# Optimization experiments

Measured on AMD Instinct MI355X. Metric: run time of the kernel, lower is better.

## Reference

```python
import jax, jax.numpy as jnp
import numpy as np

B, T, DIM, HEADS, DH = 4, 2048, 1024, 16, 64  # dh = dim // heads


def setup_inputs() -> dict:
    key = jax.random.key(0)
    k1, k2, k3 = jax.random.split(key, 3)
    x = jax.random.normal(k1, (B, T, DIM), dtype=jnp.float32)
    # nn.Linear weights, stored as [in, out] for x @ W convention
    W_qkv = jax.random.normal(k2, (DIM, 3 * HEADS * DH), dtype=jnp.float32) * (DIM ** -0.5)
    W_o = jax.random.normal(k3, (HEADS * DH, DIM), dtype=jnp.float32) * ((HEADS * DH) ** -0.5)
    return {"x": x, "W_qkv": W_qkv, "W_o": W_o}


def reference(x, W_qkv, W_o):
    b, t, _ = x.shape
    qkv = x @ W_qkv  # [b, t, 3*h*dh]
    # einops 'b t (d k h) -> k b h t d' with k=3, h=HEADS: fused axis splits as (dh, 3, h)
    qkv = qkv.reshape(b, t, DH, 3, HEADS)
    qkv = jnp.transpose(qkv, (3, 0, 4, 1, 2))  # [3, b, h, t, dh]
    q, k, v = qkv[0], qkv[1], qkv[2]
    scale = DH ** -0.5
    scores = jnp.einsum('bhid,bhjd->bhij', q, k) * scale  # [b, h, t, t]
    attn = jax.nn.softmax(scores, axis=-1)
    out = jnp.einsum('bhij,bhjd->bhid', attn, v)  # [b, h, t, dh]
    out = jnp.transpose(out, (0, 2, 1, 3)).reshape(b, t, HEADS * DH)  # 'b h t d -> b t (h d)'
    return out @ W_o
```

## Files before the change

### kernel.cpp

```cpp
#include <hip/hip_runtime.h>

typedef __bf16 bf16;
typedef __bf16 bf16x2 __attribute__((ext_vector_type(2)));
typedef __bf16 bf16x4 __attribute__((ext_vector_type(4)));
typedef __bf16 bf16x8 __attribute__((ext_vector_type(8)));
typedef float  f32x4  __attribute__((ext_vector_type(4)));
typedef unsigned int u32;
typedef unsigned int u32x2 __attribute__((ext_vector_type(2)));
typedef unsigned int u32x4 __attribute__((ext_vector_type(4)));

#define LOG2E 1.44269504088896340736f
#define EXP_SC (0.125f * LOG2E)

#if __has_builtin(__builtin_amdgcn_exp2f)
#define EXP2F(x) __builtin_amdgcn_exp2f(x)
#else
#define EXP2F(x) __builtin_exp2f(x)
#endif

__device__ __forceinline__ u32 pk_bf16(float lo, float hi) {
  u32 a = __float_as_uint(lo) + 0x8000u;
  u32 b = __float_as_uint(hi) + 0x8000u;
  return __builtin_amdgcn_perm(b, a, 0x07060302);
}
#if __has_builtin(__builtin_amdgcn_cvt_pk_bf16_f32)
__device__ __forceinline__ u32 cvtpk(float lo, float hi) {
  bf16x2 t = __builtin_amdgcn_cvt_pk_bf16_f32(lo, hi);
  return __builtin_bit_cast(u32, t);
}
#else
__device__ __forceinline__ u32 cvtpk(float lo, float hi) { return pk_bf16(lo, hi); }
#endif
__device__ __forceinline__ unsigned short bf16r(float x) {
  return (unsigned short)((__float_as_uint(x) + 0x8000u) >> 16);
}

__device__ __forceinline__ void async_ld16(void* lds, const void* g) {
  __builtin_amdgcn_global_load_lds(
      (const __attribute__((address_space(1))) void*)(g),
      (__attribute__((address_space(3))) void*)(lds),
      16, 0, 0);
}

__global__ void prep_all(const float* __restrict__ x,    bf16* __restrict__ xb,
                         const float* __restrict__ Wqkv, bf16* __restrict__ wqkvT,
                         const float* __restrict__ Wo,   bf16* __restrict__ woT) {
  __shared__ float s[12288];
  const int bid = blockIdx.x;
  const int tid = threadIdx.x;
  if (bid < 8192) {
    int i = bid * 256 + tid;
    float4 v = ((const float4*)x)[i];
    u32x2 o = { pk_bf16(v.x, v.y), pk_bf16(v.z, v.w) };
    *(u32x2*)(xb + (size_t)i * 4) = o;
  } else if (bid < 8448) {
    const int k0 = (bid - 8192) * 4;
    for (int i = tid; i < 3072; i += 256) {
      int r = i / 768, c = (i - r * 768) * 4;
      *(float4*)(s + r * 3072 + c) = *(const float4*)(Wqkv + (size_t)(k0 + r) * 3072 + c);
    }
    __syncthreads();
    for (int n = tid; n < 3072; n += 256) {
      int d = n & 63, h = (n >> 6) & 15, wch = n >> 10;
      int on = d * 48 + wch * 16 + h;
      u32x2 v = { pk_bf16(s[0 * 3072 + on], s[1 * 3072 + on]),
                  pk_bf16(s[2 * 3072 + on], s[3 * 3072 + on]) };
      *(u32x2*)(wqkvT + (size_t)n * 1024 + k0) = v;
    }
  } else {
    const int k0 = (bid - 8448) * 8;
    for (int i = tid; i < 2048; i += 256) {
      int r = i >> 8, c = (i & 255) * 4;
      *(float4*)(s + r * 1024 + c) = *(const float4*)(Wo + (size_t)(k0 + r) * 1024 + c);
    }
    __syncthreads();
    for (int n = tid; n < 1024; n += 256) {
      u32x4 v = { pk_bf16(s[0 * 1024 + n], s[1 * 1024 + n]),
                  pk_bf16(s[2 * 1024 + n], s[3 * 1024 + n]),
                  pk_bf16(s[4 * 1024 + n], s[5 * 1024 + n]),
                  pk_bf16(s[6 * 1024 + n], s[7 * 1024 + n]) };
      *(u32x4*)(woT + (size_t)n * 1024 + k0) = v;
    }
  }
}

template <int MODE>
__launch_bounds__(256, 2)
__global__ void gemm_bt(const bf16* __restrict__ A, const bf16* __restrict__ BT,
                        float* __restrict__ C, int N,
                        bf16* __restrict__ Qb, bf16* __restrict__ Kb, bf16* __restrict__ Vb) {
  constexpr int K = 1024;
  __shared__ bf16 sA[128 * 64];
  __shared__ bf16 sB[128 * 64];
  const int m0 = blockIdx.x * 128;
  const int n0 = blockIdx.y * 128;
  const int tid = threadIdx.x;
  const int lane = tid & 63;
  const int w = tid >> 6;
  const int wm = (w >> 1) * 64, wn = (w & 1) * 64;
  const int l15 = lane & 15, quad = lane >> 4;

  f32x4 acc[4][4];
  for (int i = 0; i < 4; i++)
    for (int j = 0; j < 4; j++) acc[i][j] = f32x4{0.f, 0.f, 0.f, 0.f};

  const int rT = tid >> 3;
  const int jT = (tid & 7) ^ (rT & 7);
  const bf16* gA = A  + (size_t)(m0 + rT) * K + jT * 8;
  const bf16* gB = BT + (size_t)(n0 + rT) * K + jT * 8;

  for (int k0 = 0; k0 < K; k0 += 64) {
    __syncthreads();
    for (int i = 0; i < 4; i++) {
      async_ld16((void*)(sA + (i * 256 + w * 64) * 8), gA + (size_t)i * 32 * K);
      async_ld16((void*)(sB + (i * 256 + w * 64) * 8), gB + (size_t)i * 32 * K);
    }
    gA += 64; gB += 64;
    __syncthreads();

    for (int kk = 0; kk < 2; kk++) {
      bf16x8 af[4], bfr[4];
      for (int ms = 0; ms < 4; ms++) {
        int r = wm + ms * 16 + l15;
        af[ms] = *(const bf16x8*)(sA + r * 64 + (((kk * 4 + quad) ^ (r & 7)) * 8));
      }
      for (int ns = 0; ns < 4; ns++) {
        int r = wn + ns * 16 + l15;
        bfr[ns] = *(const bf16x8*)(sB + r * 64 + (((kk * 4 + quad) ^ (r & 7)) * 8));
      }
      for (int ms = 0; ms < 4; ms++)
        for (int ns = 0; ns < 4; ns++)
          acc[ms][ns] = __builtin_amdgcn_mfma_f32_16x16x32_bf16(af[ms], bfr[ns], acc[ms][ns], 0, 0, 0);
    }
  }

  if (MODE == 0) {
    for (int ms = 0; ms < 4; ms++)
      for (int ns = 0; ns < 4; ns++)
        for (int r = 0; r < 4; r++) {
          int row = m0 + wm + ms * 16 + quad * 4 + r;
          int col = n0 + wn + ns * 16 + l15;
          C[(size_t)row * N + col] = acc[ms][ns][r];
        }
  } else {
    for (int ms = 0; ms < 4; ms++)
      for (int ns = 0; ns < 4; ns++)
        for (int r = 0; r < 4; r++) {
          int row = m0 + wm + ms * 16 + quad * 4 + r;
          int col = n0 + wn + ns * 16 + l15;
          int b = row >> 11, t = row & 2047;
          int d = col & 63, h = (col >> 6) & 15, wch = col >> 10;
          bf16* dst = (wch == 0) ? Qb : (wch == 1) ? Kb : Vb;
          float v = acc[ms][ns][r] * ((wch == 0) ? EXP_SC : 1.0f);
          ((unsigned short*)dst)[(((size_t)(b * 16 + h)) * 2048 + t) * 64 + d] = bf16r(v);
        }
  }
}

__global__ void transpose_v(const bf16* __restrict__ V, bf16* __restrict__ VT) {
  __shared__ bf16 s[64 * 66];
  const int bh = blockIdx.y;
  const int t0 = blockIdx.x * 64;
  for (int i = threadIdx.x; i < 512; i += 256) {
    int t = i >> 3, dc = (i & 7) * 8;
    bf16x8 v = *(const bf16x8*)(V + ((size_t)bh * 2048 + t0 + t) * 64 + dc);
    for (int j = 0; j < 8; j++) s[t * 66 + dc + j] = v[j];
  }
  __syncthreads();
  for (int i = threadIdx.x; i < 512; i += 256) {
    int d = i >> 3, tc = (i & 7) * 8;
    bf16x8 v;
    for (int j = 0; j < 8; j++) {
      int kp = tc + j;
      int src = ((kp & 3) * 16) + (kp >> 2);
      v[j] = s[src * 66 + d];
    }
    *(bf16x8*)(VT + ((size_t)bh * 64 + d) * 2048 + t0 + tc) = v;
  }
}

__launch_bounds__(256, 2)
__global__ void attn_fwd(const bf16* __restrict__ Q, const bf16* __restrict__ K,
                         const bf16* __restrict__ VT, bf16* __restrict__ O) {
  __shared__ bf16 sK[64 * 64];
  __shared__ bf16 sV[4][64 * 64];
  __shared__ bf16 sP[4][2][32 * 64];
  const int bh = blockIdx.x;
  const int q0 = blockIdx.y * 128;
  const int tid = threadIdx.x;
  const int lane = tid & 63, w = tid >> 6;
  const int l15 = lane & 15, quad = lane >> 4;

  bf16x8 qf[2][2];
  for (int ms = 0; ms < 2; ms++)
    for (int kk = 0; kk < 2; kk++)
      qf[ms][kk] = *(const bf16x8*)(Q + ((size_t)bh * 2048 + q0 + w * 32 + ms * 16 + l15) * 64 + kk * 32 + quad * 8);

  f32x4 oa[2][4];
  float rs[2][4];
  for (int ms = 0; ms < 2; ms++) {
    for (int ds = 0; ds < 4; ds++) oa[ms][ds] = f32x4{0.f, 0.f, 0.f, 0.f};
    for (int r = 0; r < 4; r++) rs[ms][r] = 0.f;
  }

  const int cA = w * 128 + lane;
  const int rA = cA >> 3, jA = (cA & 7) ^ (rA & 7);
  const bf16* gK = K  + ((size_t)bh * 2048 + rA) * 64 + jA * 8;
  const bf16* gV = VT + ((size_t)bh * 64 + rA) * 2048 + jA * 8;

  int kvo[4][2], pfo[2][2], pwo[2][4];
  for (int ns = 0; ns < 4; ns++)
    for (int kk = 0; kk < 2; kk++) {
      int r = ns * 16 + l15;
      kvo[ns][kk] = r * 64 + (((kk * 4 + quad) ^ (r & 7)) * 8);
    }
  for (int ms = 0; ms < 2; ms++) {
    int r = ms * 16 + l15;
    for (int kk = 0; kk < 2; kk++)
      pfo[ms][kk] = r * 64 + (((kk * 4 + quad) ^ (r & 7)) * 8);
    for (int rr = 0; rr < 4; rr++) {
      int row = ms * 16 + quad * 4 + rr;
      pwo[ms][rr] = row * 64 + (((l15 >> 1) ^ (row & 7)) * 8) + (l15 & 1) * 4;
    }
  }

  auto do_exp = [&](f32x4 (&Sp)[2][4], bf16* pw) {
    for (int ms = 0; ms < 2; ms++)
      for (int r = 0; r < 4; r++) {
        float e0 = EXP2F(Sp[ms][0][r]), e1 = EXP2F(Sp[ms][1][r]);
        float e2 = EXP2F(Sp[ms][2][r]), e3 = EXP2F(Sp[ms][3][r]);
        rs[ms][r] += (e0 + e1) + (e2 + e3);
        u32x2 pk = { cvtpk(e0, e1), cvtpk(e2, e3) };
        *(u32x2*)(pw + pwo[ms][r]) = pk;
      }
  };
  auto do_pv = [&](const bf16* pb, const bf16* vb) {
    bf16x8 vf[4][2];
    for (int ds = 0; ds < 4; ds++)
      for (int kk = 0; kk < 2; kk++)
        vf[ds][kk] = *(const bf16x8*)(vb + kvo[ds][kk]);
    for (int ms = 0; ms < 2; ms++) {
      bf16x8 pf0 = *(const bf16x8*)(pb + pfo[ms][0]);
      bf16x8 pf1 = *(const bf16x8*)(pb + pfo[ms][1]);
      for (int ds = 0; ds < 4; ds++) {
        oa[ms][ds] = __builtin_amdgcn_mfma_f32_16x16x32_bf16(pf0, vf[ds][0], oa[ms][ds], 0, 0, 0);
        oa[ms][ds] = __builtin_amdgcn_mfma_f32_16x16x32_bf16(pf1, vf[ds][1], oa[ms][ds], 0, 0, 0);
      }
    }
  };

  async_ld16((void*)(sK + w * 1024),            gK);
  async_ld16((void*)(sK + w * 1024 + 512),      gK + 512);
  async_ld16((void*)(sV[0] + w * 1024),         gV);
  async_ld16((void*)(sV[0] + w * 1024 + 512),   gV + 16384);
  gK += 4096; gV += 64;

  f32x4 SA[2][4], SB[2][4];

  auto step = [&](int t, f32x4 (&Sc)[2][4], f32x4 (&Sp)[2][4]) {
    __syncthreads();
    bf16x8 kf[4][2];
    for (int ns = 0; ns < 4; ns++)
      for (int kk = 0; kk < 2; kk++)
        kf[ns][kk] = *(const bf16x8*)(sK + kvo[ns][kk]);
    __syncthreads();
    if (t < 31) {
      bf16* vb = sV[(t + 1) & 3];
      async_ld16((void*)(sK + w * 1024),          gK);
      async_ld16((void*)(sK + w * 1024 + 512),    gK + 512);
      async_ld16((void*)(vb + w * 1024),          gV);
      async_ld16((void*)(vb + w * 1024 + 512),    gV + 16384);
      gK += 4096; gV += 64;
    }
    for (int ms = 0; ms < 2; ms++)
      for (int ns = 0; ns < 4; ns++) {
        f32x4 acc0 = f32x4{0.f, 0.f, 0.f, 0.f};
        acc0 = __builtin_amdgcn_mfma_f32_16x16x32_bf16(qf[ms][0], kf[ns][0], acc0, 0, 0, 0);
        acc0 = __builtin_amdgcn_mfma_f32_16x16x32_bf16(qf[ms][1], kf[ns][1], acc0, 0, 0, 0);
        Sc[ms][ns] = acc0;
      }
    if (t >= 1) do_exp(Sp, sP[w][(t - 1) & 1]);
    if (t >= 2) do_pv(sP[w][t & 1], sV[(t - 2) & 3]);
  };

  for (int t = 0; t < 32; t += 2) {
    step(t, SA, SB);
    step(t + 1, SB, SA);
  }
  do_exp(SB, sP[w][1]);
  do_pv(sP[w][0], sV[2]);
  do_pv(sP[w][1], sV[3]);

  const int b = bh >> 4, h = bh & 15;
  for (int ms = 0; ms < 2; ms++)
    for (int r = 0; r < 4; r++) {
      float t = rs[ms][r];
      t += __shfl_xor(t, 1, 64);
      t += __shfl_xor(t, 2, 64);
      t += __shfl_xor(t, 4, 64);
      t += __shfl_xor(t, 8, 64);
      float inv = 1.0f / t;
      int tq = q0 + w * 32 + ms * 16 + quad * 4 + r;
      for (int ds = 0; ds < 4; ds++)
        ((unsigned short*)O)[((size_t)b * 2048 + tq) * 1024 + h * 64 + ds * 16 + l15] =
            bf16r(oa[ms][ds][r] * inv);
    }
}

extern "C" void kernel_launch(void* const* d_in, const int* in_sizes, int n_in,
                              void* d_out, int out_size, void* d_ws, size_t ws_size,
                              hipStream_t stream) {
  const float* x    = (const float*)d_in[0];
  const float* Wqkv = (const float*)d_in[1];
  const float* Wo   = (const float*)d_in[2];
  float* out = (float*)d_out;
  char* ws = (char*)d_ws;

  bf16* wqkvT = (bf16*)(ws);
  bf16* woT   = (bf16*)(ws + 6291456);
  bf16* xb    = (bf16*)(ws + 8388608);
  bf16* Qb    = (bf16*)(ws + 25165824);
  bf16* Kb    = (bf16*)(ws + 41943040);
  bf16* Vb    = (bf16*)(ws + 58720256);
  bf16* VTb   = xb;
  bf16* AOb   = Vb;

  prep_all<<<8576, 256, 0, stream>>>(x, xb, Wqkv, wqkvT, Wo, woT);
  gemm_bt<1><<<dim3(64, 24), 256, 0, stream>>>(xb, wqkvT, nullptr, 3072, Qb, Kb, Vb);
  transpose_v<<<dim3(32, 64), 256, 0, stream>>>(Vb, VTb);
  attn_fwd<<<dim3(64, 16), 256, 0, stream>>>(Qb, Kb, VTb, AOb);
  gemm_bt<0><<<dim3(64, 8), 256, 0, stream>>>(AOb, woT, out, 1024, nullptr, nullptr, nullptr);
}
```

Before: 295.7 us.

## Rewrite attention with 32x32 MFMA, register-resident P, and fused V transpose

The attention kernel now computes S^T = K·Q^T with 32x32x16 MFMAs so softmax probabilities stay in registers. It packs them into PV operands via permlane32_swap instead of round-tripping through LDS, and drops the two-stage software pipeline. The QKV GEMM epilogue writes V directly in transposed layout, removing the separate transpose kernel and its memory traffic. Launch bounds rise to 3 blocks per CU, which reduces per-thread register budget and loses the exp/MFMA overlap from the old pipelining. No max-subtraction is used in either version.

```diff
diff --git a/kernel.cpp b/kernel.cpp
--- a/kernel.cpp
+++ b/kernel.cpp
@@ -5,6 +5,7 @@
 typedef __bf16 bf16x4 __attribute__((ext_vector_type(4)));
 typedef __bf16 bf16x8 __attribute__((ext_vector_type(8)));
 typedef float  f32x4  __attribute__((ext_vector_type(4)));
+typedef float  f32x16 __attribute__((ext_vector_type(16)));
 typedef unsigned int u32;
 typedef unsigned int u32x2 __attribute__((ext_vector_type(2)));
 typedef unsigned int u32x4 __attribute__((ext_vector_type(4)));
@@ -33,6 +34,13 @@
 #endif
 __device__ __forceinline__ unsigned short bf16r(float x) {
   return (unsigned short)((__float_as_uint(x) + 0x8000u) >> 16);
+}
+
+__device__ __forceinline__ f32x16 zero16() {
+  f32x16 a;
+#pragma unroll
+  for (int i = 0; i < 16; i++) a[i] = 0.f;
+  return a;
 }
 
 __device__ __forceinline__ void async_ld16(void* lds, const void* g) {
@@ -152,158 +160,138 @@
           int d = col & 63, h = (col >> 6) & 15, wch = col >> 10;
           bf16* dst = (wch == 0) ? Qb : (wch == 1) ? Kb : Vb;
           float v = acc[ms][ns][r] * ((wch == 0) ? EXP_SC : 1.0f);
-          ((unsigned short*)dst)[(((size_t)(b * 16 + h)) * 2048 + t) * 64 + d] = bf16r(v);
+          size_t idx = (wch == 2)
+              ? ((((size_t)(b * 16 + h)) * 64 + d) * 2048 + t)
+              : ((((size_t)(b * 16 + h)) * 2048 + t) * 64 + d);
+          ((unsigned short*)dst)[idx] = bf16r(v);
         }
   }
 }
 
-__global__ void transpose_v(const bf16* __restrict__ V, bf16* __restrict__ VT) {
-  __shared__ bf16 s[64 * 66];
-  const int bh = blockIdx.y;
-  const int t0 = blockIdx.x * 64;
-  for (int i = threadIdx.x; i < 512; i += 256) {
-    int t = i >> 3, dc = (i & 7) * 8;
-    bf16x8 v = *(const bf16x8*)(V + ((size_t)bh * 2048 + t0 + t) * 64 + dc);
-    for (int j = 0; j < 8; j++) s[t * 66 + dc + j] = v[j];
-  }
-  __syncthreads();
-  for (int i = threadIdx.x; i < 512; i += 256) {
-    int d = i >> 3, tc = (i & 7) * 8;
-    bf16x8 v;
-    for (int j = 0; j < 8; j++) {
-      int kp = tc + j;
-      int src = ((kp & 3) * 16) + (kp >> 2);
-      v[j] = s[src * 66 + d];
-    }
-    *(bf16x8*)(VT + ((size_t)bh * 64 + d) * 2048 + t0 + tc) = v;
-  }
-}
-
-__launch_bounds__(256, 2)
+__launch_bounds__(256, 3)
 __global__ void attn_fwd(const bf16* __restrict__ Q, const bf16* __restrict__ K,
                          const bf16* __restrict__ VT, bf16* __restrict__ O) {
   __shared__ bf16 sK[64 * 64];
   __shared__ bf16 sV[4][64 * 64];
-  __shared__ bf16 sP[4][2][32 * 64];
   const int bh = blockIdx.x;
   const int q0 = blockIdx.y * 128;
   const int tid = threadIdx.x;
   const int lane = tid & 63, w = tid >> 6;
-  const int l15 = lane & 15, quad = lane >> 4;
-
-  bf16x8 qf[2][2];
-  for (int ms = 0; ms < 2; ms++)
-    for (int kk = 0; kk < 2; kk++)
-      qf[ms][kk] = *(const bf16x8*)(Q + ((size_t)bh * 2048 + q0 + w * 32 + ms * 16 + l15) * 64 + kk * 32 + quad * 8);
-
-  f32x4 oa[2][4];
-  float rs[2][4];
-  for (int ms = 0; ms < 2; ms++) {
-    for (int ds = 0; ds < 4; ds++) oa[ms][ds] = f32x4{0.f, 0.f, 0.f, 0.f};
-    for (int r = 0; r < 4; r++) rs[ms][r] = 0.f;
-  }
+  const int l31 = lane & 31, hi = lane >> 5;
+
+  bf16x8 qf[4];
+  {
+    const bf16* qp = Q + ((size_t)bh * 2048 + q0 + w * 32 + l31) * 64 + hi * 8;
+#pragma unroll
+    for (int kq = 0; kq < 4; kq++) qf[kq] = *(const bf16x8*)(qp + kq * 16);
+  }
+
+  f32x16 oacc[2];
+  oacc[0] = zero16(); oacc[1] = zero16();
+  float rs = 0.f;
 
   const int cA = w * 128 + lane;
   const int rA = cA >> 3, jA = (cA & 7) ^ (rA & 7);
   const bf16* gK = K  + ((size_t)bh * 2048 + rA) * 64 + jA * 8;
   const bf16* gV = VT + ((size_t)bh * 64 + rA) * 2048 + jA * 8;
 
-  int kvo[4][2], pfo[2][2], pwo[2][4];
-  for (int ns = 0; ns < 4; ns++)
-    for (int kk = 0; kk < 2; kk++) {
-      int r = ns * 16 + l15;
-      kvo[ns][kk] = r * 64 + (((kk * 4 + quad) ^ (r & 7)) * 8);
-    }
-  for (int ms = 0; ms < 2; ms++) {
-    int r = ms * 16 + l15;
-    for (int kk = 0; kk < 2; kk++)
-      pfo[ms][kk] = r * 64 + (((kk * 4 + quad) ^ (r & 7)) * 8);
-    for (int rr = 0; rr < 4; rr++) {
-      int row = ms * 16 + quad * 4 + rr;
-      pwo[ms][rr] = row * 64 + (((l15 >> 1) ^ (row & 7)) * 8) + (l15 & 1) * 4;
-    }
-  }
-
-  auto do_exp = [&](f32x4 (&Sp)[2][4], bf16* pw) {
-    for (int ms = 0; ms < 2; ms++)
-      for (int r = 0; r < 4; r++) {
-        float e0 = EXP2F(Sp[ms][0][r]), e1 = EXP2F(Sp[ms][1][r]);
-        float e2 = EXP2F(Sp[ms][2][r]), e3 = EXP2F(Sp[ms][3][r]);
-        rs[ms][r] += (e0 + e1) + (e2 + e3);
-        u32x2 pk = { cvtpk(e0, e1), cvtpk(e2, e3) };
-        *(u32x2*)(pw + pwo[ms][r]) = pk;
-      }
-  };
-  auto do_pv = [&](const bf16* pb, const bf16* vb) {
-    bf16x8 vf[4][2];
-    for (int ds = 0; ds < 4; ds++)
-      for (int kk = 0; kk < 2; kk++)
-        vf[ds][kk] = *(const bf16x8*)(vb + kvo[ds][kk]);
-    for (int ms = 0; ms < 2; ms++) {
-      bf16x8 pf0 = *(const bf16x8*)(pb + pfo[ms][0]);
-      bf16x8 pf1 = *(const bf16x8*)(pb + pfo[ms][1]);
-      for (int ds = 0; ds < 4; ds++) {
-        oa[ms][ds] = __builtin_amdgcn_mfma_f32_16x16x32_bf16(pf0, vf[ds][0], oa[ms][ds], 0, 0, 0);
-        oa[ms][ds] = __builtin_amdgcn_mfma_f32_16x16x32_bf16(pf1, vf[ds][1], oa[ms][ds], 0, 0, 0);
-      }
-    }
-  };
-
-  async_ld16((void*)(sK + w * 1024),            gK);
-  async_ld16((void*)(sK + w * 1024 + 512),      gK + 512);
-  async_ld16((void*)(sV[0] + w * 1024),         gV);
-  async_ld16((void*)(sV[0] + w * 1024 + 512),   gV + 16384);
+  int fo[2][4];
+#pragma unroll
+  for (int sub = 0; sub < 2; sub++)
+#pragma unroll
+    for (int st = 0; st < 4; st++) {
+      int r = sub * 32 + l31;
+      fo[sub][st] = r * 64 + (((st * 2 + hi) ^ (r & 7)) * 8);
+    }
+
+  async_ld16((void*)(sK + w * 1024),           gK);
+  async_ld16((void*)(sK + w * 1024 + 512),     gK + 512);
+  async_ld16((void*)(sV[0] + w * 1024),        gV);
+  async_ld16((void*)(sV[0] + w * 1024 + 512),  gV + 16384);
   gK += 4096; gV += 64;
 
-  f32x4 SA[2][4], SB[2][4];
-
-  auto step = [&](int t, f32x4 (&Sc)[2][4], f32x4 (&Sp)[2][4]) {
-    __syncthreads();
-    bf16x8 kf[4][2];
-    for (int ns = 0; ns < 4; ns++)
-      for (int kk = 0; kk < 2; kk++)
-        kf[ns][kk] = *(const bf16x8*)(sK + kvo[ns][kk]);
-    __syncthreads();
+  for (int t = 0; t < 32; t++) {
+    __syncthreads();
+    bf16x8 kf[2][4];
+#pragma unroll
+    for (int ks = 0; ks < 2; ks++)
+#pragma unroll
+      for (int kq = 0; kq < 4; kq++)
+        kf[ks][kq] = *(const bf16x8*)(sK + fo[ks][kq]);
+    __syncthreads();
+    const bf16* vb = sV[t & 3];
     if (t < 31) {
-      bf16* vb = sV[(t + 1) & 3];
+      bf16* vn = (bf16*)sV[(t + 1) & 3];
       async_ld16((void*)(sK + w * 1024),          gK);
       async_ld16((void*)(sK + w * 1024 + 512),    gK + 512);
-      async_ld16((void*)(vb + w * 1024),          gV);
-      async_ld16((void*)(vb + w * 1024 + 512),    gV + 16384);
+      async_ld16((void*)(vn + w * 1024),          gV);
+      async_ld16((void*)(vn + w * 1024 + 512),    gV + 16384);
       gK += 4096; gV += 64;
     }
-    for (int ms = 0; ms < 2; ms++)
-      for (int ns = 0; ns < 4; ns++) {
-        f32x4 acc0 = f32x4{0.f, 0.f, 0.f, 0.f};
-        acc0 = __builtin_amdgcn_mfma_f32_16x16x32_bf16(qf[ms][0], kf[ns][0], acc0, 0, 0, 0);
-        acc0 = __builtin_amdgcn_mfma_f32_16x16x32_bf16(qf[ms][1], kf[ns][1], acc0, 0, 0, 0);
-        Sc[ms][ns] = acc0;
-      }
-    if (t >= 1) do_exp(Sp, sP[w][(t - 1) & 1]);
-    if (t >= 2) do_pv(sP[w][t & 1], sV[(t - 2) & 3]);
-  };
-
-  for (int t = 0; t < 32; t += 2) {
-    step(t, SA, SB);
-    step(t + 1, SB, SA);
-  }
-  do_exp(SB, sP[w][1]);
-  do_pv(sP[w][0], sV[2]);
-  do_pv(sP[w][1], sV[3]);
-
+
+    f32x16 S[2];
+#pragma unroll
+    for (int ks = 0; ks < 2; ks++) {
+      f32x16 a = zero16();
+      a = __builtin_amdgcn_mfma_f32_32x32x16_bf16(kf[ks][0], qf[0], a, 0, 0, 0);
+      a = __builtin_amdgcn_mfma_f32_32x32x16_bf16(kf[ks][1], qf[1], a, 0, 0, 0);
+      a = __builtin_amdgcn_mfma_f32_32x32x16_bf16(kf[ks][2], qf[2], a, 0, 0, 0);
+      a = __builtin_amdgcn_mfma_f32_32x32x16_bf16(kf[ks][3], qf[3], a, 0, 0, 0);
+      S[ks] = a;
+    }
+
+    bf16x8 vf[2][4];
+#pragma unroll
+    for (int ds = 0; ds < 2; ds++)
+#pragma unroll
+      for (int kk = 0; kk < 4; kk++)
+        vf[ds][kk] = *(const bf16x8*)(vb + fo[ds][kk]);
+
+    bf16x8 F[4];
+#pragma unroll
+    for (int ks = 0; ks < 2; ks++) {
+      float p[16];
+#pragma unroll
+      for (int r = 0; r < 16; r++) p[r] = EXP2F(S[ks][r]);
+      rs += (((p[0] + p[1]) + (p[2] + p[3])) + ((p[4] + p[5]) + (p[6] + p[7])))
+          + (((p[8] + p[9]) + (p[10] + p[11])) + ((p[12] + p[13]) + (p[14] + p[15])));
+      u32 c0 = cvtpk(p[0],  p[1]),  c1 = cvtpk(p[2],  p[3]);
+      u32 c2 = cvtpk(p[4],  p[5]),  c3 = cvtpk(p[6],  p[7]);
+      u32 c4 = cvtpk(p[8],  p[9]),  c5 = cvtpk(p[10], p[11]);
+      u32 c6 = cvtpk(p[12], p[13]), c7 = cvtpk(p[14], p[15]);
+      asm("v_permlane32_swap_b32 %0, %1" : "+v"(c0), "+v"(c2));
+      asm("v_permlane32_swap_b32 %0, %1" : "+v"(c1), "+v"(c3));
+      asm("v_permlane32_swap_b32 %0, %1" : "+v"(c4), "+v"(c6));
+      asm("v_permlane32_swap_b32 %0, %1" : "+v"(c5), "+v"(c7));
+      u32x4 f0 = { c0, c1, c2, c3 };
+      u32x4 f1 = { c4, c5, c6, c7 };
+      F[ks * 2 + 0] = __builtin_bit_cast(bf16x8, f0);
+      F[ks * 2 + 1] = __builtin_bit_cast(bf16x8, f1);
+    }
+
+#pragma unroll
+    for (int ds = 0; ds < 2; ds++) {
+      f32x16 a = oacc[ds];
+      a = __builtin_amdgcn_mfma_f32_32x32x16_bf16(vf[ds][0], F[0], a, 0, 0, 0);
+      a = __builtin_amdgcn_mfma_f32_32x32x16_bf16(vf[ds][1], F[1], a, 0, 0, 0);
+      a = __builtin_amdgcn_mfma_f32_32x32x16_bf16(vf[ds][2], F[2], a, 0, 0, 0);
+      a = __builtin_amdgcn_mfma_f32_32x32x16_bf16(vf[ds][3], F[3], a, 0, 0, 0);
+      oacc[ds] = a;
+    }
+  }
+
+  float rt = rs + __shfl_xor(rs, 32, 64);
+  float inv = 1.0f / rt;
   const int b = bh >> 4, h = bh & 15;
-  for (int ms = 0; ms < 2; ms++)
-    for (int r = 0; r < 4; r++) {
-      float t = rs[ms][r];
-      t += __shfl_xor(t, 1, 64);
-      t += __shfl_xor(t, 2, 64);
-      t += __shfl_xor(t, 4, 64);
-      t += __shfl_xor(t, 8, 64);
-      float inv = 1.0f / t;
-      int tq = q0 + w * 32 + ms * 16 + quad * 4 + r;
-      for (int ds = 0; ds < 4; ds++)
-        ((unsigned short*)O)[((size_t)b * 2048 + tq) * 1024 + h * 64 + ds * 16 + l15] =
-            bf16r(oa[ms][ds][r] * inv);
+  const int trow = q0 + w * 32 + l31;
+#pragma unroll
+  for (int ds = 0; ds < 2; ds++)
+#pragma unroll
+    for (int g = 0; g < 4; g++) {
+      int d = ds * 32 + g * 8 + hi * 4;
+      u32x2 pkv = { cvtpk(oacc[ds][g * 4 + 0] * inv, oacc[ds][g * 4 + 1] * inv),
+                    cvtpk(oacc[ds][g * 4 + 2] * inv, oacc[ds][g * 4 + 3] * inv) };
+      *(u32x2*)(O + ((size_t)b * 2048 + trow) * 1024 + h * 64 + d) = pkv;
     }
 }
 
@@ -321,13 +309,11 @@
   bf16* xb    = (bf16*)(ws + 8388608);
   bf16* Qb    = (bf16*)(ws + 25165824);
   bf16* Kb    = (bf16*)(ws + 41943040);
-  bf16* Vb    = (bf16*)(ws + 58720256);
-  bf16* VTb   = xb;
-  bf16* AOb   = Vb;
+  bf16* VTb   = (bf16*)(ws + 58720256);
+  bf16* AOb   = xb;
 
   prep_all<<<8576, 256, 0, stream>>>(x, xb, Wqkv, wqkvT, Wo, woT);
-  gemm_bt<1><<<dim3(64, 24), 256, 0, stream>>>(xb, wqkvT, nullptr, 3072, Qb, Kb, Vb);
-  transpose_v<<<dim3(32, 64), 256, 0, stream>>>(Vb, VTb);
+  gemm_bt<1><<<dim3(64, 24), 256, 0, stream>>>(xb, wqkvT, nullptr, 3072, Qb, Kb, VTb);
   attn_fwd<<<dim3(64, 16), 256, 0, stream>>>(Qb, Kb, VTb, AOb);
   gemm_bt<0><<<dim3(64, 8), 256, 0, stream>>>(AOb, woT, out, 1024, nullptr, nullptr, nullptr);
 }
```

Result: faster. 281.5 us (-4.8%).
